# Kernel tuning notes

Measured on AMD Instinct MI355X. Metric: run time of the kernel, lower is better.

The kernel has to match this reference:

```python
import jax, jax.numpy as jnp
import numpy as np


def _gcn_conv(x, W, b, src, dst, norm, n_nodes):
    # PyG GCNConv: h = x @ W, then symmetric-normalized aggregation, then + b
    h = x @ W                                   # [N, F_out]
    msg = h[src] * norm[:, None]                # gather + scale, [E', F_out]
    agg = jax.ops.segment_sum(msg, dst, num_segments=n_nodes)
    return agg + b


def _norm_and_loops(edge_index, n_nodes):
    # add self-loops, compute D^{-1/2} (A+I) D^{-1/2} edge weights
    loop = jnp.arange(n_nodes, dtype=edge_index.dtype)
    src = jnp.concatenate([edge_index[0], loop])
    dst = jnp.concatenate([edge_index[1], loop])
    deg = jax.ops.segment_sum(jnp.ones_like(dst, dtype=jnp.float32), dst,
                              num_segments=n_nodes)
    dinv = jnp.where(deg > 0, jax.lax.rsqrt(deg), 0.0)
    norm = dinv[src] * dinv[dst]
    return src, dst, norm


def setup_inputs() -> dict:
    key = jax.random.key(0)
    ks = jax.random.split(key, 4)
    N, E, n_latent, n_dim = 50000, 800000, 128, 128
    hidden = 2 * n_latent
    x = jax.random.normal(ks[0], (N, n_latent), dtype=jnp.float32)
    edge_index = jax.random.randint(ks[1], (2, E), 0, N, dtype=jnp.int64)
    W1 = jax.random.normal(ks[2], (n_latent, hidden), dtype=jnp.float32) / np.sqrt(n_latent)
    b1 = jnp.zeros((hidden,), dtype=jnp.float32)
    W2 = jax.random.normal(ks[3], (hidden, n_dim), dtype=jnp.float32) / np.sqrt(hidden)
    b2 = jnp.zeros((n_dim,), dtype=jnp.float32)
    return {"x": x, "edge_index": edge_index, "W1": W1, "b1": b1,
            "W2": W2, "b2": b2}


def reference(x, edge_index, W1, b1, W2, b2):
    n_nodes = x.shape[0]
    src, dst, norm = _norm_and_loops(edge_index, n_nodes)
    z1 = jax.nn.relu(_gcn_conv(x, W1, b1, src, dst, norm, n_nodes))
    z2 = _gcn_conv(z1, W2, b2, src, dst, norm, n_nodes)
    return z2
```

## Files before the change

### kernel.cpp

```cpp
#include <hip/hip_runtime.h>


constexpr int F = 128;
constexpr int HID = 256;
constexpr int ECHUNK = 8192;

typedef __attribute__((ext_vector_type(8))) _Float16 f16x8;
typedef __attribute__((ext_vector_type(4))) _Float16 f16x4;
typedef __attribute__((ext_vector_type(2))) _Float16 f16x2;
typedef __attribute__((ext_vector_type(4))) float f32x4;

__global__ __launch_bounds__(256) void k_bzero(unsigned* bcnt) {
  bcnt[threadIdx.x] = 0u;
}

__global__ __launch_bounds__(256) void k_binc(const int* __restrict__ dst,
                                              unsigned* __restrict__ bcnt, int E) {
  __shared__ unsigned hist[256];
  int tid = threadIdx.x;
  hist[tid] = 0u;
  __syncthreads();
  int i0 = blockIdx.x * ECHUNK;
  int i1 = min(i0 + ECHUNK, E);
  for (int i = i0 + tid; i < i1; i += 256)
    atomicAdd(&hist[((unsigned)dst[i]) >> 8], 1u);
  __syncthreads();
  unsigned c = hist[tid];
  if (c) atomicAdd(&bcnt[tid], c);
}

__global__ __launch_bounds__(256) void k_bscan(const unsigned* __restrict__ bcnt,
                                               unsigned* __restrict__ bbase,
                                               unsigned* __restrict__ bcur,
                                               int* __restrict__ rowptr,
                                               int P, int N, int E) {
  __shared__ unsigned wsum[4];
  int tid = threadIdx.x;
  unsigned v = (tid < P) ? bcnt[tid] : 0u;
  unsigned sv = v;
#pragma unroll
  for (int off = 1; off < 64; off <<= 1) {
    unsigned t = __shfl_up(sv, off);
    if ((tid & 63) >= off) sv += t;
  }
  int w = tid >> 6;
  if ((tid & 63) == 63) wsum[w] = sv;
  __syncthreads();
  unsigned wpre = 0;
  for (int k = 0; k < w; ++k) wpre += wsum[k];
  unsigned excl = wpre + sv - v;
  if (tid < P) {
    bbase[tid] = excl;
    bcur[tid] = excl;
  }
  if (tid == P - 1) bbase[P] = excl + v;
  if (tid == 0) rowptr[N] = E;
}

__global__ __launch_bounds__(256) void k_binscat(const int* __restrict__ src,
                                                 const int* __restrict__ dst,
                                                 unsigned* __restrict__ bcur,
                                                 unsigned* __restrict__ packed, int E) {
  __shared__ unsigned hist[256];
  __shared__ unsigned basel[256];
  int tid = threadIdx.x;
  hist[tid] = 0u;
  __syncthreads();
  int i0 = blockIdx.x * ECHUNK;
  int i1 = min(i0 + ECHUNK, E);
  for (int i = i0 + tid; i < i1; i += 256)
    atomicAdd(&hist[((unsigned)dst[i]) >> 8], 1u);
  __syncthreads();
  unsigned c = hist[tid];
  if (c) basel[tid] = atomicAdd(&bcur[tid], c);
  __syncthreads();
  hist[tid] = 0u;
  __syncthreads();
  for (int i = i0 + tid; i < i1; i += 256) {
    unsigned d = (unsigned)dst[i];
    unsigned b = d >> 8;
    unsigned pos = basel[b] + atomicAdd(&hist[b], 1u);
    packed[pos] = ((unsigned)src[i]) | ((d & 255u) << 16);
  }
}

__global__ __launch_bounds__(256) void k_bcsr(const unsigned* __restrict__ packed,
                                              const unsigned* __restrict__ bbase,
                                              unsigned* __restrict__ deg,
                                              int* __restrict__ rowptr,
                                              int* __restrict__ esrc, int N) {
  __shared__ unsigned hist[256];
  __shared__ unsigned rowloc[256];
  __shared__ unsigned cur[256];
  __shared__ unsigned wsum[4];
  int tid = threadIdx.x, b = blockIdx.x;
  int e0 = (int)bbase[b], e1 = (int)bbase[b + 1];
  hist[tid] = 0u;
  __syncthreads();
  for (int i = e0 + tid; i < e1; i += 256)
    atomicAdd(&hist[packed[i] >> 16], 1u);
  __syncthreads();
  unsigned v = hist[tid];
  unsigned sv = v;
#pragma unroll
  for (int off = 1; off < 64; off <<= 1) {
    unsigned t = __shfl_up(sv, off);
    if ((tid & 63) >= off) sv += t;
  }
  int w = tid >> 6;
  if ((tid & 63) == 63) wsum[w] = sv;
  __syncthreads();
  unsigned wpre = 0;
  for (int k = 0; k < w; ++k) wpre += wsum[k];
  unsigned excl = wpre + sv - v;
  int node = b * 256 + tid;
  if (node < N) {
    deg[node] = v;
    rowptr[node] = e0 + (int)excl;
  }
  rowloc[tid] = (unsigned)e0 + excl;
  cur[tid] = 0u;
  __syncthreads();
  for (int i = e0 + tid; i < e1; i += 256) {
    unsigned pk = packed[i];
    unsigned dl = pk >> 16;
    unsigned pos = rowloc[dl] + atomicAdd(&cur[dl], 1u);
    esrc[pos] = (int)(pk & 0xffffu);
  }
}

__global__ __launch_bounds__(256) void k_dinv(const unsigned* __restrict__ deg,
                                              float* dinv, int N) {
  int i = blockIdx.x * 256 + threadIdx.x;
  if (i < N) dinv[i] = rsqrtf((float)deg[i] + 1.0f);
}

__global__ __launch_bounds__(256) void k_toh(const float* __restrict__ in,
                                             _Float16* __restrict__ outp, int n4) {
  int i = blockIdx.x * 256 + threadIdx.x;
  if (i >= n4) return;
  float4 v = ((const float4*)in)[i];
  f16x4 o;
  o.x = (_Float16)v.x; o.y = (_Float16)v.y;
  o.z = (_Float16)v.z; o.w = (_Float16)v.w;
  ((f16x4*)outp)[i] = o;
}

__global__ __launch_bounds__(256) void k_wcvt(const float* __restrict__ W,
                                              _Float16* __restrict__ Wt,
                                              int K, int Nn) {
  int idx = blockIdx.x * 256 + threadIdx.x;
  if (idx >= K * Nn) return;
  int k = idx / Nn, n = idx - k * Nn;
  Wt[n * K + k] = (_Float16)W[idx];
}

__global__ __launch_bounds__(256) void k_agg1(const int* __restrict__ rowptr,
                                              const int* __restrict__ esrc,
                                              const float* __restrict__ dinv,
                                              const float* __restrict__ xf,
                                              const _Float16* __restrict__ xh,
                                              _Float16* __restrict__ outp, int N) {
  int node = blockIdx.x * 4 + (threadIdx.x >> 6);
  int lane = threadIdx.x & 63;
  if (node >= N) return;
  float di = dinv[node];
  float w0 = di * di;
  float2 acc = ((const float2*)(xf + (size_t)node * F))[lane];
  acc.x *= w0; acc.y *= w0;
  int beg = rowptr[node], end = rowptr[node + 1];
  for (int b = beg; b < end; b += 64) {
    int n = min(64, end - b);
    int s = 0;
    float w = 0.f;
    if (lane < n) {
      s = esrc[b + lane];
      w = dinv[s] * di;
    }
    int t = 0;
    for (; t + 3 < n; t += 4) {
      int s0 = __shfl(s, t), s1 = __shfl(s, t + 1);
      int s2 = __shfl(s, t + 2), s3 = __shfl(s, t + 3);
      float wa = __shfl(w, t), wb = __shfl(w, t + 1);
      float wc = __shfl(w, t + 2), wd = __shfl(w, t + 3);
      f16x2 v0 = ((const f16x2*)(xh + (size_t)s0 * F))[lane];
      f16x2 v1 = ((const f16x2*)(xh + (size_t)s1 * F))[lane];
      f16x2 v2 = ((const f16x2*)(xh + (size_t)s2 * F))[lane];
      f16x2 v3 = ((const f16x2*)(xh + (size_t)s3 * F))[lane];
      acc.x += (float)v0.x * wa; acc.y += (float)v0.y * wa;
      acc.x += (float)v1.x * wb; acc.y += (float)v1.y * wb;
      acc.x += (float)v2.x * wc; acc.y += (float)v2.y * wc;
      acc.x += (float)v3.x * wd; acc.y += (float)v3.y * wd;
    }
    for (; t < n; ++t) {
      int s0 = __shfl(s, t);
      float wa = __shfl(w, t);
      f16x2 v0 = ((const f16x2*)(xh + (size_t)s0 * F))[lane];
      acc.x += (float)v0.x * wa; acc.y += (float)v0.y * wa;
    }
  }
  f16x2 ov;
  ov.x = (_Float16)acc.x;
  ov.y = (_Float16)acc.y;
  ((f16x2*)(outp + (size_t)node * F))[lane] = ov;
}

__global__ __launch_bounds__(256) void k_agg_out(const int* __restrict__ rowptr,
                                                 const int* __restrict__ esrc,
                                                 const float* __restrict__ dinv,
                                                 const _Float16* __restrict__ hb,
                                                 const float* __restrict__ bias,
                                                 float* __restrict__ outp, int N) {
  int node = blockIdx.x * 4 + (threadIdx.x >> 6);
  int lane = threadIdx.x & 63;
  if (node >= N) return;
  float di = dinv[node];
  float w0 = di * di;
  f16x2 sv2 = ((const f16x2*)(hb + (size_t)node * F))[lane];
  float2 bb = ((const float2*)bias)[lane];
  float2 acc;
  acc.x = (float)sv2.x * w0 + bb.x;
  acc.y = (float)sv2.y * w0 + bb.y;
  int beg = rowptr[node], end = rowptr[node + 1];
  for (int b = beg; b < end; b += 64) {
    int n = min(64, end - b);
    int s = 0;
    float w = 0.f;
    if (lane < n) {
      s = esrc[b + lane];
      w = dinv[s] * di;
    }
    int t = 0;
    for (; t + 3 < n; t += 4) {
      int s0 = __shfl(s, t), s1 = __shfl(s, t + 1);
      int s2 = __shfl(s, t + 2), s3 = __shfl(s, t + 3);
      float wa = __shfl(w, t), wb = __shfl(w, t + 1);
      float wc = __shfl(w, t + 2), wd = __shfl(w, t + 3);
      f16x2 v0 = ((const f16x2*)(hb + (size_t)s0 * F))[lane];
      f16x2 v1 = ((const f16x2*)(hb + (size_t)s1 * F))[lane];
      f16x2 v2 = ((const f16x2*)(hb + (size_t)s2 * F))[lane];
      f16x2 v3 = ((const f16x2*)(hb + (size_t)s3 * F))[lane];
      acc.x += (float)v0.x * wa; acc.y += (float)v0.y * wa;
      acc.x += (float)v1.x * wb; acc.y += (float)v1.y * wb;
      acc.x += (float)v2.x * wc; acc.y += (float)v2.y * wc;
      acc.x += (float)v3.x * wd; acc.y += (float)v3.y * wd;
    }
    for (; t < n; ++t) {
      int s0 = __shfl(s, t);
      float wa = __shfl(w, t);
      f16x2 v0 = ((const f16x2*)(hb + (size_t)s0 * F))[lane];
      acc.x += (float)v0.x * wa; acc.y += (float)v0.y * wa;
    }
  }
  ((float2*)(outp + (size_t)node * F))[lane] = acc;
}

__global__ __launch_bounds__(256) void k_gemm1(const _Float16* __restrict__ A,
                                               const _Float16* __restrict__ Bt,
                                               const float* __restrict__ bias,
                                               _Float16* __restrict__ C, int M) {
  __shared__ _Float16 AL[64 * 128];
  int tid = threadIdx.x;
  int lane = tid & 63, wid = tid >> 6;
  int row0 = blockIdx.x * 64;
  int col0 = blockIdx.y * 128;

#pragma unroll
  for (int i = 0; i < 4; ++i) {
    int g = i * 256 + tid;
    int r = g >> 4, gi = g & 15;
    int o = r * 128 + ((gi ^ (r & 7)) * 8);
    size_t go = (size_t)(row0 + r) * 128 + gi * 8;
    *(f16x8*)&AL[o] = *(const f16x8*)&A[go];
  }
  __syncthreads();

  f32x4 acc[4][2] = {};
#pragma unroll
  for (int ks = 0; ks < 4; ++ks) {
    f16x8 ah[4], bh[2];
#pragma unroll
    for (int mf = 0; mf < 4; ++mf) {
      int r = mf * 16 + (lane & 15);
      int g = ks * 4 + (lane >> 4);
      int o = r * 128 + ((g ^ (r & 7)) * 8);
      ah[mf] = *(const f16x8*)&AL[o];
    }
#pragma unroll
    for (int nf = 0; nf < 2; ++nf) {
      int c = col0 + wid * 32 + nf * 16 + (lane & 15);
      size_t o = (size_t)c * 128 + ks * 32 + (lane >> 4) * 8;
      bh[nf] = *(const f16x8*)&Bt[o];
    }
#pragma unroll
    for (int mf = 0; mf < 4; ++mf)
#pragma unroll
      for (int nf = 0; nf < 2; ++nf)
        acc[mf][nf] = __builtin_amdgcn_mfma_f32_16x16x32_f16(
            ah[mf], bh[nf], acc[mf][nf], 0, 0, 0);
  }

#pragma unroll
  for (int mf = 0; mf < 4; ++mf) {
    int r0 = row0 + mf * 16 + (lane >> 4) * 4;
#pragma unroll
    for (int nf = 0; nf < 2; ++nf) {
      int c = col0 + wid * 32 + nf * 16 + (lane & 15);
      float bv = bias[c];
#pragma unroll
      for (int r = 0; r < 4; ++r) {
        if (r0 + r < M) {
          float v = fmaxf(acc[mf][nf][r] + bv, 0.f);
          C[(size_t)(r0 + r) * HID + c] = (_Float16)v;
        }
      }
    }
  }
}

__global__ __launch_bounds__(256) void k_gemm2(const _Float16* __restrict__ Z,
                                               const _Float16* __restrict__ Bt,
                                               _Float16* __restrict__ C, int M) {
  __shared__ _Float16 ZL[64 * 256];
  int tid = threadIdx.x;
  int lane = tid & 63, wid = tid >> 6;
  int row0 = blockIdx.x * 64;

#pragma unroll
  for (int i = 0; i < 8; ++i) {
    int g = i * 256 + tid;
    int r = g >> 5, gi = g & 31;
    int o = r * 256 + ((gi ^ (r & 7)) * 8);
    size_t go = (size_t)(row0 + r) * 256 + gi * 8;
    *(f16x8*)&ZL[o] = *(const f16x8*)&Z[go];
  }
  __syncthreads();

  f32x4 acc[4][2] = {};
#pragma unroll
  for (int ks = 0; ks < 8; ++ks) {
    f16x8 ah[4], bh[2];
#pragma unroll
    for (int mf = 0; mf < 4; ++mf) {
      int r = mf * 16 + (lane & 15);
      int g = ks * 4 + (lane >> 4);
      int o = r * 256 + ((g ^ (r & 7)) * 8);
      ah[mf] = *(const f16x8*)&ZL[o];
    }
#pragma unroll
    for (int nf = 0; nf < 2; ++nf) {
      int c = wid * 32 + nf * 16 + (lane & 15);
      size_t o = (size_t)c * 256 + ks * 32 + (lane >> 4) * 8;
      bh[nf] = *(const f16x8*)&Bt[o];
    }
#pragma unroll
    for (int mf = 0; mf < 4; ++mf)
#pragma unroll
      for (int nf = 0; nf < 2; ++nf)
        acc[mf][nf] = __builtin_amdgcn_mfma_f32_16x16x32_f16(
            ah[mf], bh[nf], acc[mf][nf], 0, 0, 0);
  }

#pragma unroll
  for (int mf = 0; mf < 4; ++mf) {
    int r0 = row0 + mf * 16 + (lane >> 4) * 4;
#pragma unroll
    for (int nf = 0; nf < 2; ++nf) {
      int c = wid * 32 + nf * 16 + (lane & 15);
#pragma unroll
      for (int r = 0; r < 4; ++r)
        if (r0 + r < M) C[(size_t)(r0 + r) * F + c] = (_Float16)acc[mf][nf][r];
    }
  }
}

extern "C" void kernel_launch(void* const* d_in, const int* in_sizes, int n_in,
                              void* d_out, int out_size, void* d_ws, size_t ws_size,
                              hipStream_t stream) {
  const float* x = (const float*)d_in[0];
  const int* ei = (const int*)d_in[1];
  const float* W1 = (const float*)d_in[2];
  const float* b1 = (const float*)d_in[3];
  const float* W2 = (const float*)d_in[4];
  const float* b2 = (const float*)d_in[5];
  float* out = (float*)d_out;

  int N = in_sizes[0] / F;
  int E = in_sizes[1] / 2;
  const int* src = ei;
  const int* dst = ei + E;
  int P = (N + 255) / 256;

  char* ws = (char*)d_ws;
  size_t off = 0;
  auto allocB = [&](size_t bytes) {
    void* p = ws + off;
    off += ((bytes + 255) & ~(size_t)255);
    return p;
  };
  unsigned* deg = (unsigned*)allocB((size_t)N * 4);
  float* dinv = (float*)allocB((size_t)N * 4);
  int* rowptr = (int*)allocB(((size_t)N + 1) * 4);
  unsigned* bcnt = (unsigned*)allocB(256 * 4);
  unsigned* bbase = (unsigned*)allocB(257 * 4);
  unsigned* bcur = (unsigned*)allocB(256 * 4);
  unsigned* packed = (unsigned*)allocB((size_t)E * 4);
  int* esrc = (int*)allocB((size_t)E * 4);
  _Float16* xh = (_Float16*)allocB((size_t)N * F * 2);
  _Float16* agg = (_Float16*)allocB((size_t)(N + 64) * F * 2);
  _Float16* z1 = (_Float16*)allocB((size_t)(N + 64) * HID * 2);
  _Float16* w1t = (_Float16*)allocB((size_t)F * HID * 2);
  _Float16* w2t = (_Float16*)allocB((size_t)HID * F * 2);
  _Float16* h2 = agg;

  int nbN = (N + 255) / 256;
  int nbW = (F * HID + 255) / 256;
  int nbX = (N * F / 4 + 255) / 256;
  int nbC = (E + ECHUNK - 1) / ECHUNK;

  k_wcvt<<<nbW, 256, 0, stream>>>(W1, w1t, F, HID);
  k_wcvt<<<nbW, 256, 0, stream>>>(W2, w2t, HID, F);
  k_toh<<<nbX, 256, 0, stream>>>(x, xh, N * F / 4);

  k_bzero<<<1, 256, 0, stream>>>(bcnt);
  k_binc<<<nbC, 256, 0, stream>>>(dst, bcnt, E);
  k_bscan<<<1, 256, 0, stream>>>(bcnt, bbase, bcur, rowptr, P, N, E);
  k_binscat<<<nbC, 256, 0, stream>>>(src, dst, bcur, packed, E);
  k_bcsr<<<P, 256, 0, stream>>>(packed, bbase, deg, rowptr, esrc, N);
  k_dinv<<<nbN, 256, 0, stream>>>(deg, dinv, N);

  int nbAgg = (N + 3) / 4;
  int mb = (N + 63) / 64;

  k_agg1<<<nbAgg, 256, 0, stream>>>(rowptr, esrc, dinv, x, xh, agg, N);
  dim3 g1(mb, 2);
  k_gemm1<<<g1, 256, 0, stream>>>(agg, w1t, b1, z1, N);

  k_gemm2<<<mb, 256, 0, stream>>>(z1, w2t, h2, N);
  k_agg_out<<<nbAgg, 256, 0, stream>>>(rowptr, esrc, dinv, h2, b2, out, N);
}
```

Measured before the change: 173.3 us.

## Reuse bin histograms, fold dinv into CSR build, unroll gathers, widen gemm1 tile

k_binc now stores each chunk's per-bin histogram so k_binscat no longer recounts the destination array. The degree-to-dinv step is computed inside k_bcsr, which removes one kernel launch and the deg buffer. The aggregation loops gather 8 neighbours per iteration instead of 4, giving more loads in flight. gemm1 now has each block compute all 256 output columns, halving the grid and re-staging the A tile half as often, at the cost of more accumulator registers.

```diff
diff --git a/kernel.cpp b/kernel.cpp
--- a/kernel.cpp
+++ b/kernel.cpp
@@ -15,7 +15,8 @@
 }
 
 __global__ __launch_bounds__(256) void k_binc(const int* __restrict__ dst,
-                                              unsigned* __restrict__ bcnt, int E) {
+                                              unsigned* __restrict__ bcnt,
+                                              unsigned* __restrict__ bhist, int E) {
   __shared__ unsigned hist[256];
   int tid = threadIdx.x;
   hist[tid] = 0u;
@@ -26,6 +27,7 @@
     atomicAdd(&hist[((unsigned)dst[i]) >> 8], 1u);
   __syncthreads();
   unsigned c = hist[tid];
+  bhist[blockIdx.x * 256 + tid] = c;
   if (c) atomicAdd(&bcnt[tid], c);
 }
 
@@ -59,23 +61,18 @@
 
 __global__ __launch_bounds__(256) void k_binscat(const int* __restrict__ src,
                                                  const int* __restrict__ dst,
+                                                 const unsigned* __restrict__ bhist,
                                                  unsigned* __restrict__ bcur,
                                                  unsigned* __restrict__ packed, int E) {
   __shared__ unsigned hist[256];
   __shared__ unsigned basel[256];
   int tid = threadIdx.x;
+  unsigned c = bhist[blockIdx.x * 256 + tid];
+  if (c) basel[tid] = atomicAdd(&bcur[tid], c);
   hist[tid] = 0u;
   __syncthreads();
   int i0 = blockIdx.x * ECHUNK;
   int i1 = min(i0 + ECHUNK, E);
-  for (int i = i0 + tid; i < i1; i += 256)
-    atomicAdd(&hist[((unsigned)dst[i]) >> 8], 1u);
-  __syncthreads();
-  unsigned c = hist[tid];
-  if (c) basel[tid] = atomicAdd(&bcur[tid], c);
-  __syncthreads();
-  hist[tid] = 0u;
-  __syncthreads();
   for (int i = i0 + tid; i < i1; i += 256) {
     unsigned d = (unsigned)dst[i];
     unsigned b = d >> 8;
@@ -86,7 +83,7 @@
 
 __global__ __launch_bounds__(256) void k_bcsr(const unsigned* __restrict__ packed,
                                               const unsigned* __restrict__ bbase,
-                                              unsigned* __restrict__ deg,
+                                              float* __restrict__ dinv,
                                               int* __restrict__ rowptr,
                                               int* __restrict__ esrc, int N) {
   __shared__ unsigned hist[256];
@@ -115,7 +112,7 @@
   unsigned excl = wpre + sv - v;
   int node = b * 256 + tid;
   if (node < N) {
-    deg[node] = v;
+    dinv[node] = rsqrtf((float)v + 1.0f);
     rowptr[node] = e0 + (int)excl;
   }
   rowloc[tid] = (unsigned)e0 + excl;
@@ -127,12 +124,6 @@
     unsigned pos = rowloc[dl] + atomicAdd(&cur[dl], 1u);
     esrc[pos] = (int)(pk & 0xffffu);
   }
-}
-
-__global__ __launch_bounds__(256) void k_dinv(const unsigned* __restrict__ deg,
-                                              float* dinv, int N) {
-  int i = blockIdx.x * 256 + threadIdx.x;
-  if (i < N) dinv[i] = rsqrtf((float)deg[i] + 1.0f);
 }
 
 __global__ __launch_bounds__(256) void k_toh(const float* __restrict__ in,
@@ -178,25 +169,30 @@
       w = dinv[s] * di;
     }
     int t = 0;
-    for (; t + 3 < n; t += 4) {
-      int s0 = __shfl(s, t), s1 = __shfl(s, t + 1);
-      int s2 = __shfl(s, t + 2), s3 = __shfl(s, t + 3);
-      float wa = __shfl(w, t), wb = __shfl(w, t + 1);
-      float wc = __shfl(w, t + 2), wd = __shfl(w, t + 3);
-      f16x2 v0 = ((const f16x2*)(xh + (size_t)s0 * F))[lane];
-      f16x2 v1 = ((const f16x2*)(xh + (size_t)s1 * F))[lane];
-      f16x2 v2 = ((const f16x2*)(xh + (size_t)s2 * F))[lane];
-      f16x2 v3 = ((const f16x2*)(xh + (size_t)s3 * F))[lane];
-      acc.x += (float)v0.x * wa; acc.y += (float)v0.y * wa;
-      acc.x += (float)v1.x * wb; acc.y += (float)v1.y * wb;
-      acc.x += (float)v2.x * wc; acc.y += (float)v2.y * wc;
-      acc.x += (float)v3.x * wd; acc.y += (float)v3.y * wd;
+    for (; t + 7 < n; t += 8) {
+      int ss[8];
+      float wz[8];
+#pragma unroll
+      for (int j = 0; j < 8; ++j) {
+        ss[j] = __shfl(s, t + j);
+        wz[j] = __shfl(w, t + j);
+      }
+      f16x2 vv[8];
+#pragma unroll
+      for (int j = 0; j < 8; ++j)
+        vv[j] = ((const f16x2*)(xh + (size_t)ss[j] * F))[lane];
+#pragma unroll
+      for (int j = 0; j < 8; ++j) {
+        acc.x += (float)vv[j].x * wz[j];
+        acc.y += (float)vv[j].y * wz[j];
+      }
     }
     for (; t < n; ++t) {
       int s0 = __shfl(s, t);
       float wa = __shfl(w, t);
       f16x2 v0 = ((const f16x2*)(xh + (size_t)s0 * F))[lane];
-      acc.x += (float)v0.x * wa; acc.y += (float)v0.y * wa;
+      acc.x += (float)v0.x * wa;
+      acc.y += (float)v0.y * wa;
     }
   }
   f16x2 ov;
@@ -231,25 +227,30 @@
       w = dinv[s] * di;
     }
     int t = 0;
-    for (; t + 3 < n; t += 4) {
-      int s0 = __shfl(s, t), s1 = __shfl(s, t + 1);
-      int s2 = __shfl(s, t + 2), s3 = __shfl(s, t + 3);
-      float wa = __shfl(w, t), wb = __shfl(w, t + 1);
-      float wc = __shfl(w, t + 2), wd = __shfl(w, t + 3);
-      f16x2 v0 = ((const f16x2*)(hb + (size_t)s0 * F))[lane];
-      f16x2 v1 = ((const f16x2*)(hb + (size_t)s1 * F))[lane];
-      f16x2 v2 = ((const f16x2*)(hb + (size_t)s2 * F))[lane];
-      f16x2 v3 = ((const f16x2*)(hb + (size_t)s3 * F))[lane];
-      acc.x += (float)v0.x * wa; acc.y += (float)v0.y * wa;
-      acc.x += (float)v1.x * wb; acc.y += (float)v1.y * wb;
-      acc.x += (float)v2.x * wc; acc.y += (float)v2.y * wc;
-      acc.x += (float)v3.x * wd; acc.y += (float)v3.y * wd;
+    for (; t + 7 < n; t += 8) {
+      int ss[8];
+      float wz[8];
+#pragma unroll
+      for (int j = 0; j < 8; ++j) {
+        ss[j] = __shfl(s, t + j);
+        wz[j] = __shfl(w, t + j);
+      }
+      f16x2 vv[8];
+#pragma unroll
+      for (int j = 0; j < 8; ++j)
+        vv[j] = ((const f16x2*)(hb + (size_t)ss[j] * F))[lane];
+#pragma unroll
+      for (int j = 0; j < 8; ++j) {
+        acc.x += (float)vv[j].x * wz[j];
+        acc.y += (float)vv[j].y * wz[j];
+      }
     }
     for (; t < n; ++t) {
       int s0 = __shfl(s, t);
       float wa = __shfl(w, t);
       f16x2 v0 = ((const f16x2*)(hb + (size_t)s0 * F))[lane];
-      acc.x += (float)v0.x * wa; acc.y += (float)v0.y * wa;
+      acc.x += (float)v0.x * wa;
+      acc.y += (float)v0.y * wa;
     }
   }
   ((float2*)(outp + (size_t)node * F))[lane] = acc;
@@ -263,7 +264,6 @@
   int tid = threadIdx.x;
   int lane = tid & 63, wid = tid >> 6;
   int row0 = blockIdx.x * 64;
-  int col0 = blockIdx.y * 128;
 
 #pragma unroll
   for (int i = 0; i < 4; ++i) {
@@ -275,10 +275,10 @@
   }
   __syncthreads();
 
-  f32x4 acc[4][2] = {};
+  f32x4 acc[4][4] = {};
 #pragma unroll
   for (int ks = 0; ks < 4; ++ks) {
-    f16x8 ah[4], bh[2];
+    f16x8 ah[4], bh[4];
 #pragma unroll
     for (int mf = 0; mf < 4; ++mf) {
       int r = mf * 16 + (lane & 15);
@@ -287,15 +287,15 @@
       ah[mf] = *(const f16x8*)&AL[o];
     }
 #pragma unroll
-    for (int nf = 0; nf < 2; ++nf) {
-      int c = col0 + wid * 32 + nf * 16 + (lane & 15);
+    for (int nf = 0; nf < 4; ++nf) {
+      int c = wid * 64 + nf * 16 + (lane & 15);
       size_t o = (size_t)c * 128 + ks * 32 + (lane >> 4) * 8;
       bh[nf] = *(const f16x8*)&Bt[o];
     }
 #pragma unroll
     for (int mf = 0; mf < 4; ++mf)
 #pragma unroll
-      for (int nf = 0; nf < 2; ++nf)
+      for (int nf = 0; nf < 4; ++nf)
         acc[mf][nf] = __builtin_amdgcn_mfma_f32_16x16x32_f16(
             ah[mf], bh[nf], acc[mf][nf], 0, 0, 0);
   }
@@ -304,8 +304,8 @@
   for (int mf = 0; mf < 4; ++mf) {
     int r0 = row0 + mf * 16 + (lane >> 4) * 4;
 #pragma unroll
-    for (int nf = 0; nf < 2; ++nf) {
-      int c = col0 + wid * 32 + nf * 16 + (lane & 15);
+    for (int nf = 0; nf < 4; ++nf) {
+      int c = wid * 64 + nf * 16 + (lane & 15);
       float bv = bias[c];
 #pragma unroll
       for (int r = 0; r < 4; ++r) {
@@ -390,6 +390,7 @@
   const int* src = ei;
   const int* dst = ei + E;
   int P = (N + 255) / 256;
+  int nbC = (E + ECHUNK - 1) / ECHUNK;
 
   char* ws = (char*)d_ws;
   size_t off = 0;
@@ -398,12 +399,12 @@
     off += ((bytes + 255) & ~(size_t)255);
     return p;
   };
-  unsigned* deg = (unsigned*)allocB((size_t)N * 4);
   float* dinv = (float*)allocB((size_t)N * 4);
   int* rowptr = (int*)allocB(((size_t)N + 1) * 4);
   unsigned* bcnt = (unsigned*)allocB(256 * 4);
   unsigned* bbase = (unsigned*)allocB(257 * 4);
   unsigned* bcur = (unsigned*)allocB(256 * 4);
+  unsigned* bhist = (unsigned*)allocB((size_t)nbC * 256 * 4);
   unsigned* packed = (unsigned*)allocB((size_t)E * 4);
   int* esrc = (int*)allocB((size_t)E * 4);
   _Float16* xh = (_Float16*)allocB((size_t)N * F * 2);
@@ -413,28 +414,24 @@
   _Float16* w2t = (_Float16*)allocB((size_t)HID * F * 2);
   _Float16* h2 = agg;
 
-  int nbN = (N + 255) / 256;
   int nbW = (F * HID + 255) / 256;
   int nbX = (N * F / 4 + 255) / 256;
-  int nbC = (E + ECHUNK - 1) / ECHUNK;
 
   k_wcvt<<<nbW, 256, 0, stream>>>(W1, w1t, F, HID);
   k_wcvt<<<nbW, 256, 0, stream>>>(W2, w2t, HID, F);
   k_toh<<<nbX, 256, 0, stream>>>(x, xh, N * F / 4);
 
   k_bzero<<<1, 256, 0, stream>>>(bcnt);
-  k_binc<<<nbC, 256, 0, stream>>>(dst, bcnt, E);
+  k_binc<<<nbC, 256, 0, stream>>>(dst, bcnt, bhist, E);
   k_bscan<<<1, 256, 0, stream>>>(bcnt, bbase, bcur, rowptr, P, N, E);
-  k_binscat<<<nbC, 256, 0, stream>>>(src, dst, bcur, packed, E);
-  k_bcsr<<<P, 256, 0, stream>>>(packed, bbase, deg, rowptr, esrc, N);
-  k_dinv<<<nbN, 256, 0, stream>>>(deg, dinv, N);
+  k_binscat<<<nbC, 256, 0, stream>>>(src, dst, bhist, bcur, packed, E);
+  k_bcsr<<<P, 256, 0, stream>>>(packed, bbase, dinv, rowptr, esrc, N);
 
   int nbAgg = (N + 3) / 4;
   int mb = (N + 63) / 64;
 
   k_agg1<<<nbAgg, 256, 0, stream>>>(rowptr, esrc, dinv, x, xh, agg, N);
-  dim3 g1(mb, 2);
-  k_gemm1<<<g1, 256, 0, stream>>>(agg, w1t, b1, z1, N);
+  k_gemm1<<<mb, 256, 0, stream>>>(agg, w1t, b1, z1, N);
 
   k_gemm2<<<mb, 256, 0, stream>>>(z1, w2t, h2, N);
   k_agg_out<<<nbAgg, 256, 0, stream>>>(rowptr, esrc, dinv, h2, b2, out, N);
```

Measured after the change: 170.4 us. About the same (-1.7%).
